# Kernel optimization log

Measured on AMD Instinct MI355X. Metric: run time of the kernel, lower is better.

Reference implementation:

```python
import jax, jax.numpy as jnp
import numpy as np

B, T, D = 4, 4096, 1024
H, K, V = 16, 64, 64
EPS = 1e-6


def setup_inputs() -> dict:
    key = jax.random.key(0)
    ks = jax.random.split(key, 7)
    s = 0.02
    return {
        "x": jax.random.normal(ks[0], (B, T, D), dtype=jnp.float32),
        "norm_w": jnp.ones((D,), dtype=jnp.float32),
        "Wk": jax.random.normal(ks[1], (H * K, D), dtype=jnp.float32) * s,
        "Wv": jax.random.normal(ks[2], (H * V, D), dtype=jnp.float32) * s,
        "Wo": jax.random.normal(ks[3], (D, H * V), dtype=jnp.float32) * s,
        "Wb": jax.random.normal(ks[4], (H, D), dtype=jnp.float32) * s,
        "bb": jnp.full((H,), -2.0, dtype=jnp.float32),
        "Wg": jax.random.normal(ks[5], (H, D), dtype=jnp.float32) * s,
        "bg": jnp.full((H,), 2.0, dtype=jnp.float32),
    }


def reference(x, norm_w, Wk, Wv, Wo, Wb, bb, Wg, bg):
    # RMSNorm
    rms = jnp.sqrt(jnp.mean(x * x, axis=-1, keepdims=True) + EPS)
    xn = x / rms * norm_w  # [B,T,D]

    k = (xn @ Wk.T).reshape(B, T, H, K)
    v = (xn @ Wv.T).reshape(B, T, H, V)
    # L2-normalize keys (F.normalize, eps=1e-12)
    kn = jnp.linalg.norm(k, axis=-1, keepdims=True)
    k = k / jnp.maximum(kn, 1e-12)

    beta = jax.nn.sigmoid(xn @ Wb.T + bb)  # [B,T,H]
    g = jax.nn.sigmoid(xn @ Wg.T + bg)     # [B,T,H]

    # time-major for scan
    k_t = jnp.transpose(k, (1, 0, 2, 3))       # [T,B,H,K]
    v_t = jnpp = jnp.transpose(v, (1, 0, 2, 3))  # [T,B,H,V]
    b_t = jnp.transpose(beta, (1, 0, 2))       # [T,B,H]
    g_t = jnp.transpose(g, (1, 0, 2))          # [T,B,H]

    state0 = jnp.zeros((B, H, K, V), dtype=jnp.float32)

    def step(state, inp):
        kt, vt, bt, gt = inp  # [B,H,K],[B,H,V],[B,H],[B,H]
        pred = jnp.einsum('bhkv,bhk->bhv', state, kt)
        err = vt - pred
        state = gt[..., None, None] * state + bt[..., None, None] * (kt[..., :, None] * err[..., None, :])
        out_t = jnp.einsum('bhkv,bhk->bhv', state, kt)
        return state, out_t

    final_state, out = jax.lax.scan(step, state0, (k_t, v_t, b_t, g_t))
    out = jnp.transpose(out, (1, 0, 2, 3)).reshape(B, T, H * V)  # [B,T,H*V]
    y = x + out @ Wo.T
    return y
```

## Files before the change

### kernel.cpp

```cpp
#include <hip/hip_runtime.h>
#include <stdint.h>

#define B_ 4
#define T_ 4096
#define D_ 1024
#define H_ 16
#define NPAD 2176
#define ROWS (B_*T_)

typedef __bf16 bf16x8 __attribute__((ext_vector_type(8)));
typedef float  f32x4  __attribute__((ext_vector_type(4)));
typedef unsigned short u16;
typedef u16 u16x8 __attribute__((ext_vector_type(8)));
typedef u16 u16x4 __attribute__((ext_vector_type(4)));

__device__ __forceinline__ float bf2f(u16 u){
  union { unsigned int i; float f; } x; x.i = ((unsigned int)u) << 16; return x.f;
}
__device__ __forceinline__ u16 f2bf(float f){
  union { float f; unsigned int i; } x; x.f = f;
  unsigned int r = x.i + 0x7fffu + ((x.i >> 16) & 1u);
  return (u16)(r >> 16);
}
__device__ __forceinline__ bf16x8 as_bf(u16x8 v){ union{u16x8 u; bf16x8 b;} x; x.u = v; return x.b; }

__device__ __forceinline__ void gload_lds16(const u16* g, u16* l){
  __builtin_amdgcn_global_load_lds(
      (const __attribute__((address_space(1))) unsigned int*)g,
      (__attribute__((address_space(3))) unsigned int*)l, 16, 0, 0);
}

__global__ __launch_bounds__(256) void prep_w(
    const float* __restrict__ Wk, const float* __restrict__ Wv,
    const float* __restrict__ Wb, const float* __restrict__ Wg,
    const float* __restrict__ Wo, u16* __restrict__ Wcomb, u16* __restrict__ Wob)
{
  long i = (long)blockIdx.x * 256 + threadIdx.x;
  const long tot1 = (long)NPAD * D_;
  if (i < tot1) {
    long n = i >> 10, d = i & 1023;
    float v;
    if      (n < 1024) v = Wk[n * 1024 + d];
    else if (n < 2048) v = Wv[(n - 1024) * 1024 + d];
    else if (n < 2064) v = Wb[(n - 2048) * 1024 + d];
    else if (n < 2080) v = Wg[(n - 2064) * 1024 + d];
    else               v = 0.f;
    Wcomb[i] = f2bf(v);
  } else {
    long j = i - tot1;
    Wob[j] = f2bf(Wo[j]);
  }
}

__global__ __launch_bounds__(256) void rmsnorm_k(
    const float* __restrict__ x, const float* __restrict__ w, u16* __restrict__ xn)
{
  long row = blockIdx.x;
  int tid = threadIdx.x;
  int l = tid & 63, wv = tid >> 6;
  f32x4 v = ((const f32x4*)(x + row * D_))[tid];
  float ss = v[0]*v[0] + v[1]*v[1] + v[2]*v[2] + v[3]*v[3];
  #pragma unroll
  for (int m = 1; m < 64; m <<= 1) ss += __shfl_xor(ss, m, 64);
  __shared__ float red[4];
  if (l == 0) red[wv] = ss;
  __syncthreads();
  float tot = red[0] + red[1] + red[2] + red[3];
  float inv = rsqrtf(tot * (1.f / (float)D_) + 1e-6f);
  f32x4 wv4 = ((const f32x4*)w)[tid];
  u16x4 o;
  o[0] = f2bf(v[0] * inv * wv4[0]);
  o[1] = f2bf(v[1] * inv * wv4[1]);
  o[2] = f2bf(v[2] * inv * wv4[2]);
  o[3] = f2bf(v[3] * inv * wv4[3]);
  ((u16x4*)(xn + row * D_))[tid] = o;
}

template<int RESID, int OUTF32>
__global__ __launch_bounds__(256) void gemm_nt(
    const u16* __restrict__ A, const u16* __restrict__ Bm,
    u16* __restrict__ Cb, float* __restrict__ Cf, const float* __restrict__ resid,
    int M, int N, int Kd)
{
  __shared__ __align__(16) u16 Als[128 * 32];
  __shared__ __align__(16) u16 Bls[128 * 32];
  const int tid = threadIdx.x;
  const int w = tid >> 6, l = tid & 63;
  const int wr = w >> 1, wc = w & 1;
  const int lm = l & 15, lq = l >> 4;

  unsigned bid = blockIdx.y * gridDim.x + blockIdx.x;
  unsigned nwg = gridDim.x * gridDim.y;
  unsigned cpx = nwg >> 3;
  unsigned swz = (bid & 7) * cpx + (bid >> 3);
  const long bm0 = (long)(swz / gridDim.x) * 128;
  const long bn0 = (long)(swz % gridDim.x) * 128;

  f32x4 zero4 = {0.f, 0.f, 0.f, 0.f};
  f32x4 acc[4][4];
  #pragma unroll
  for (int i = 0; i < 4; i++)
    #pragma unroll
    for (int j = 0; j < 4; j++) acc[i][j] = zero4;

  for (int kk = 0; kk < Kd; kk += 32) {
    __syncthreads();
    #pragma unroll
    for (int it = 0; it < 2; it++) {
      int c = tid + it * 256;
      int r = c >> 2, kb = c & 3;
      const u16* ga = A  + (bm0 + r) * Kd + kk + kb * 8;
      const u16* gb = Bm + (bn0 + r) * Kd + kk + kb * 8;
      gload_lds16(ga, Als + (it * 256 + w * 64) * 8);
      gload_lds16(gb, Bls + (it * 256 + w * 64) * 8);
    }
    __syncthreads();
    bf16x8 af[4], bfr[4];
    #pragma unroll
    for (int f = 0; f < 4; f++)
      af[f] = *(const bf16x8*)(Als + (wr * 64 + f * 16 + lm) * 32 + lq * 8);
    #pragma unroll
    for (int f = 0; f < 4; f++)
      bfr[f] = *(const bf16x8*)(Bls + (wc * 64 + f * 16 + lm) * 32 + lq * 8);
    #pragma unroll
    for (int i = 0; i < 4; i++)
      #pragma unroll
      for (int j = 0; j < 4; j++)
        acc[i][j] = __builtin_amdgcn_mfma_f32_16x16x32_bf16(af[i], bfr[j], acc[i][j], 0, 0, 0);
  }

  #pragma unroll
  for (int i = 0; i < 4; i++) {
    #pragma unroll
    for (int r = 0; r < 4; r++) {
      long m = bm0 + wr * 64 + i * 16 + lq * 4 + r;
      #pragma unroll
      for (int j = 0; j < 4; j++) {
        long n = bn0 + wc * 64 + j * 16 + lm;
        float val = acc[i][j][r];
        if (RESID) val += resid[m * N + n];
        if (OUTF32) Cf[m * N + n] = val;
        else        Cb[m * N + n] = f2bf(val);
      }
    }
  }
}

__global__ __launch_bounds__(64) void postproc(
    u16* __restrict__ kv, const float* __restrict__ bb, const float* __restrict__ bg,
    float* __restrict__ bArr, float* __restrict__ gArr)
{
  long row = blockIdx.x;
  int l = threadIdx.x;
  u16* rp = kv + row * NPAD;
  #pragma unroll
  for (int h = 0; h < 16; h++) {
    float xk = bf2f(rp[h * 64 + l]);
    float ss = xk * xk;
    #pragma unroll
    for (int m = 1; m < 64; m <<= 1) ss += __shfl_xor(ss, m, 64);
    float inv = 1.f / fmaxf(sqrtf(ss), 1e-12f);
    rp[h * 64 + l] = f2bf(xk * inv);
  }
  if (l < 32) {
    int hh = l & 15;
    float val = bf2f(rp[2048 + l]) + ((l < 16) ? bb[hh] : bg[hh]);
    float s = 1.f / (1.f + expf(-val));
    float* dst = (l < 16) ? bArr : gArr;
    long b = row >> 12;
    long t = row & 4095;
    dst[(b * H_ + hh) * (long)T_ + t] = s;
  }
}

__device__ __forceinline__ void mm64(const u16* Ab, const u16* Bb,
                                     int lm, int lq, int wr, int wc, f32x4 acc[2][2])
{
  #pragma unroll
  for (int ks = 0; ks < 2; ++ks) {
    bf16x8 af[2], bfr[2];
    #pragma unroll
    for (int mi = 0; mi < 2; ++mi)
      af[mi] = *(const bf16x8*)(Ab + (wr*32 + mi*16 + lm)*72 + ks*32 + lq*8);
    #pragma unroll
    for (int ni = 0; ni < 2; ++ni)
      bfr[ni] = *(const bf16x8*)(Bb + (wc*32 + ni*16 + lm)*72 + ks*32 + lq*8);
    #pragma unroll
    for (int mi = 0; mi < 2; ++mi)
      #pragma unroll
      for (int ni = 0; ni < 2; ++ni)
        acc[mi][ni] = __builtin_amdgcn_mfma_f32_16x16x32_bf16(af[mi], bfr[ni], acc[mi][ni], 0, 0, 0);
  }
}

__global__ __launch_bounds__(256) void chunk1(
    u16* __restrict__ kv, const float* __restrict__ bArr, const float* __restrict__ gArr,
    u16* __restrict__ p1buf, u16* __restrict__ r1buf)
{
  __shared__ __align__(16) u16 Kb[64*72];
  __shared__ __align__(16) u16 Utb[128*72];
  __shared__ __align__(16) u16 LpI[64*72];
  __shared__ __align__(16) u16 Abf[64*72];
  __shared__ __align__(16) float Ad[4*16*21];
  __shared__ float aLS[64], ainvLS[64], bLS[64], bapLS[64];
  __shared__ float aCsh;

  const int tid = threadIdx.x;
  const int w = tid >> 6, l = tid & 63;
  const int lm = l & 15, lq = l >> 4;
  const int wr = w >> 1, wc = w & 1;
  const int bh = blockIdx.x & 63, ch = blockIdx.x >> 6;
  const int b = bh >> 4, h = bh & 15;

  const u16* kbase = kv + ((long)b*T_ + ch*64)*NPAD + h*64;
  const u16* vbase = kbase + 1024;

  #pragma unroll
  for (int it = 0; it < 2; ++it) {
    int c = tid + it*256;
    int r = c >> 3, seg = (c & 7)*8;
    *(u16x8*)(Kb  + r*72 + seg) = *(const u16x8*)(kbase + (long)r*NPAD + seg);
    *(u16x8*)(Utb + r*72 + seg) = *(const u16x8*)(vbase + (long)r*NPAD + seg);
  }
  #pragma unroll
  for (int z = 0; z < 8; ++z) {
    int idx = tid + z*256;
    int rr = idx >> 5, wd = idx & 31;
    ((unsigned int*)(Utb + (64 + rr)*72))[wd] = 0u;
  }
  if (tid < 64) {
    float gv = gArr[(long)bh*T_ + ch*64 + tid];
    float bv = bArr[(long)bh*T_ + ch*64 + tid];
    float av = gv;
    #pragma unroll
    for (int off = 1; off < 64; off <<= 1) {
      float o = __shfl_up(av, off, 64);
      if (tid >= off) av *= o;
    }
    float ap = __shfl_up(av, 1, 64);
    if (tid == 0) ap = 1.f;
    float aC = __shfl(av, 63, 64);
    aLS[tid] = av; ainvLS[tid] = 1.f/av; bLS[tid] = bv; bapLS[tid] = bv*ap;
    if (tid == 0) aCsh = aC;
  }
  __syncthreads();

  f32x4 gf[2][2];
  #pragma unroll
  for (int mi = 0; mi < 2; ++mi)
    #pragma unroll
    for (int ni = 0; ni < 2; ++ni) gf[mi][ni] = f32x4{0.f,0.f,0.f,0.f};
  mm64(Kb, Kb, lm, lq, wr, wc, gf);

  float wv_[4][2][4];
  #pragma unroll
  for (int bi = 0; bi < 4; ++bi)
    #pragma unroll
    for (int ni = 0; ni < 2; ++ni) {
      int col = w*32 + ni*16 + lm;
      #pragma unroll
      for (int r = 0; r < 4; ++r) {
        int row = bi*16 + lq*4 + r;
        float sv = (col < 64) ? bf2f(Utb[row*72 + col]) : bf2f(Kb[row*72 + (col - 64)]);
        float coef = (col < 64) ? bLS[row] : bapLS[row];
        wv_[bi][ni][r] = coef * sv;
      }
    }

  #pragma unroll
  for (int mi = 0; mi < 2; ++mi)
    #pragma unroll
    for (int ni = 0; ni < 2; ++ni)
      #pragma unroll
      for (int r = 0; r < 4; ++r) {
        int row = wr*32 + mi*16 + lq*4 + r, col = wc*32 + ni*16 + lm;
        float gvl = gf[mi][ni][r];
        int rb = row >> 4, cb = col >> 4;
        Abf[row*72 + col] = f2bf((rb > cb) ? bapLS[row]*ainvLS[col]*gvl : 0.f);
        if (rb == cb)
          Ad[(rb*16 + (row & 15))*21 + (col & 15)] =
              ((col & 15) < (row & 15)) ? bapLS[row]*ainvLS[col]*gvl : 0.f;
        LpI[row*72 + col] = f2bf((col < row) ? aLS[row]*ainvLS[col]*gvl
                                             : ((col == row) ? 1.f : 0.f));
      }
  __syncthreads();

  #pragma unroll
  for (int bi = 0; bi < 4; ++bi) {
    if (bi > 0) {
      f32x4 corr[2] = { f32x4{0.f,0.f,0.f,0.f}, f32x4{0.f,0.f,0.f,0.f} };
      const int nks = (bi*16 + 31) >> 5;
      #pragma unroll
      for (int ks = 0; ks < 2; ++ks) {
        if (ks < nks) {
          bf16x8 afr = *(const bf16x8*)(Abf + (bi*16 + lm)*72 + ks*32 + lq*8);
          #pragma unroll
          for (int ni = 0; ni < 2; ++ni) {
            bf16x8 bfr = *(const bf16x8*)(Utb + (w*32 + ni*16 + lm)*72 + ks*32 + lq*8);
            corr[ni] = __builtin_amdgcn_mfma_f32_16x16x32_bf16(afr, bfr, corr[ni], 0, 0, 0);
          }
        }
      }
      #pragma unroll
      for (int ni = 0; ni < 2; ++ni)
        #pragma unroll
        for (int r = 0; r < 4; ++r) wv_[bi][ni][r] -= corr[ni][r];
    }
    #pragma unroll
    for (int i = 0; i < 16; ++i) {
      int src = ((i >> 2) << 4) | lm;
      float u0 = __shfl(wv_[bi][0][i & 3], src, 64);
      float u1 = __shfl(wv_[bi][1][i & 3], src, 64);
      #pragma unroll
      for (int r = 0; r < 4; ++r) {
        float ad = Ad[(bi*16 + lq*4 + r)*21 + i];
        wv_[bi][0][r] = fmaf(-ad, u0, wv_[bi][0][r]);
        wv_[bi][1][r] = fmaf(-ad, u1, wv_[bi][1][r]);
      }
    }
    #pragma unroll
    for (int ni = 0; ni < 2; ++ni) {
      int col = w*32 + ni*16 + lm;
      #pragma unroll
      for (int r = 0; r < 4; ++r)
        Utb[col*72 + bi*16 + lq*4 + r] = f2bf(wv_[bi][ni][r]);
    }
  }
  __syncthreads();

  const long pr_base = (((long)bh*64 + ch)*64);
  u16* qdst = kv + ((long)b*T_ + ch*64)*NPAD + h*64;
  u16* mdst = qdst + 1024;
  f32x4 acc[2][2];

  #pragma unroll
  for (int mi = 0; mi < 2; ++mi)
    #pragma unroll
    for (int ni = 0; ni < 2; ++ni) acc[mi][ni] = f32x4{0.f,0.f,0.f,0.f};
  mm64(Utb, LpI, lm, lq, wr, wc, acc);
  #pragma unroll
  for (int mi = 0; mi < 2; ++mi)
    #pragma unroll
    for (int ni = 0; ni < 2; ++ni)
      #pragma unroll
      for (int r = 0; r < 4; ++r) {
        int row = wr*32 + mi*16 + lq*4 + r, col = wc*32 + ni*16 + lm;
        p1buf[(pr_base + row)*64 + col] = f2bf(acc[mi][ni][r]);
      }

  #pragma unroll
  for (int mi = 0; mi < 2; ++mi)
    #pragma unroll
    for (int ni = 0; ni < 2; ++ni) acc[mi][ni] = f32x4{0.f,0.f,0.f,0.f};
  mm64(LpI, Utb + 64*72, lm, lq, wr, wc, acc);
  #pragma unroll
  for (int mi = 0; mi < 2; ++mi)
    #pragma unroll
    for (int ni = 0; ni < 2; ++ni)
      #pragma unroll
      for (int r = 0; r < 4; ++r) {
        int row = wr*32 + mi*16 + lq*4 + r, col = wc*32 + ni*16 + lm;
        float val = aLS[row]*bf2f(Kb[row*72 + col]) - acc[mi][ni][r];
        qdst[(long)row*NPAD + col] = f2bf(val);
      }

  {
    int kk_ = tid >> 2, sb = (tid & 3) * 16;
    float aC = aCsh;
    #pragma unroll
    for (int s5 = 0; s5 < 16; ++s5) {
      int s = sb + s5;
      Abf[kk_*72 + s] = f2bf(aC * ainvLS[s] * bf2f(Kb[s*72 + kk_]));
    }
  }
  __syncthreads();

  #pragma unroll
  for (int mi = 0; mi < 2; ++mi)
    #pragma unroll
    for (int ni = 0; ni < 2; ++ni) acc[mi][ni] = f32x4{0.f,0.f,0.f,0.f};
  mm64(Utb, Abf, lm, lq, wr, wc, acc);
  #pragma unroll
  for (int mi = 0; mi < 2; ++mi)
    #pragma unroll
    for (int ni = 0; ni < 2; ++ni)
      #pragma unroll
      for (int r = 0; r < 4; ++r) {
        int row = wr*32 + mi*16 + lq*4 + r, col = wc*32 + ni*16 + lm;
        r1buf[(pr_base + row)*64 + col] = f2bf(acc[mi][ni][r]);
      }

  #pragma unroll
  for (int mi = 0; mi < 2; ++mi)
    #pragma unroll
    for (int ni = 0; ni < 2; ++ni) acc[mi][ni] = f32x4{0.f,0.f,0.f,0.f};
  mm64(Abf, Utb + 64*72, lm, lq, wr, wc, acc);
  #pragma unroll
  for (int mi = 0; mi < 2; ++mi)
    #pragma unroll
    for (int ni = 0; ni < 2; ++ni)
      #pragma unroll
      for (int r = 0; r < 4; ++r) {
        int row = wr*32 + mi*16 + lq*4 + r, col = wc*32 + ni*16 + lm;
        float val = ((row == col) ? aCsh : 0.f) - acc[mi][ni][r];
        mdst[(long)row*NPAD + col] = f2bf(val);
      }
}

struct PF { u16x8 qf0, qf1, mf0, mf1; u16 p1[4]; u16 r1[4]; };

__global__ __launch_bounds__(256) void chunk2(
    const u16* __restrict__ kv, const u16* __restrict__ p1buf, const u16* __restrict__ r1buf,
    u16* __restrict__ outb)
{
  __shared__ __align__(16) u16 Zb[16*72];
  __shared__ __align__(16) u16 ot[64*24];
  const int tid = threadIdx.x;
  const int wcv = tid >> 6, l = tid & 63;
  const int lm = l & 15, lq = l >> 4;
  const int bh = blockIdx.x & 63, vg = blockIdx.x >> 6;
  const int b = bh >> 4, h = bh & 15;

  for (int idx = tid; idx < 16*72/2; idx += 256) ((unsigned int*)Zb)[idx] = 0u;

  const u16* pbase = p1buf + (long)bh*64*4096;
  const u16* rbase = r1buf + (long)bh*64*4096;

  auto LOADPF = [&](int ch, PF& p){
    long rq = ((long)b*T_ + ch*64 + wcv*16 + lm)*NPAD + h*64 + lq*8;
    p.qf0 = *(const u16x8*)(kv + rq);
    p.qf1 = *(const u16x8*)(kv + rq + 32);
    p.mf0 = *(const u16x8*)(kv + rq + 1024);
    p.mf1 = *(const u16x8*)(kv + rq + 1024 + 32);
    #pragma unroll
    for (int r = 0; r < 4; ++r) {
      long pv = (long)ch*4096 + (vg*16 + lq*4 + r)*64 + wcv*16 + lm;
      p.p1[r] = pbase[pv];
      p.r1[r] = rbase[pv];
    }
  };

  PF A, Bp;
  LOADPF(0, A);
  __syncthreads();

  auto STEP = [&](int ch, PF& use, PF& pre){
    bf16x8 za0 = *(const bf16x8*)(Zb + lm*72 + lq*8);
    bf16x8 za1 = *(const bf16x8*)(Zb + lm*72 + 32 + lq*8);
    if (ch < 63) LOADPF(ch + 1, pre);
    f32x4 accO = { bf2f(use.p1[0]), bf2f(use.p1[1]), bf2f(use.p1[2]), bf2f(use.p1[3]) };
    accO = __builtin_amdgcn_mfma_f32_16x16x32_bf16(za0, as_bf(use.qf0), accO, 0, 0, 0);
    accO = __builtin_amdgcn_mfma_f32_16x16x32_bf16(za1, as_bf(use.qf1), accO, 0, 0, 0);
    f32x4 accS = { bf2f(use.r1[0]), bf2f(use.r1[1]), bf2f(use.r1[2]), bf2f(use.r1[3]) };
    accS = __builtin_amdgcn_mfma_f32_16x16x32_bf16(za0, as_bf(use.mf0), accS, 0, 0, 0);
    accS = __builtin_amdgcn_mfma_f32_16x16x32_bf16(za1, as_bf(use.mf1), accS, 0, 0, 0);
    #pragma unroll
    for (int r = 0; r < 4; ++r) ot[(wcv*16 + lm)*24 + lq*4 + r] = f2bf(accO[r]);
    __syncthreads();
    #pragma unroll
    for (int r = 0; r < 4; ++r) Zb[(lq*4 + r)*72 + wcv*16 + lm] = f2bf(accS[r]);
    {
      int i2 = tid >> 2, q4 = tid & 3;
      u16x4 ov = *(const u16x4*)(ot + i2*24 + q4*4);
      *(u16x4*)(outb + ((long)b*T_ + ch*64 + i2)*D_ + h*64 + vg*16 + q4*4) = ov;
    }
    __syncthreads();
  };

  for (int c2 = 0; c2 < 32; ++c2) {
    STEP(2*c2,     A, Bp);
    STEP(2*c2 + 1, Bp, A);
  }
}

extern "C" void kernel_launch(void* const* d_in, const int* in_sizes, int n_in,
                              void* d_out, int out_size, void* d_ws, size_t ws_size,
                              hipStream_t stream) {
  const float* x     = (const float*)d_in[0];
  const float* normw = (const float*)d_in[1];
  const float* Wk    = (const float*)d_in[2];
  const float* Wv    = (const float*)d_in[3];
  const float* Wo    = (const float*)d_in[4];
  const float* Wb    = (const float*)d_in[5];
  const float* bb    = (const float*)d_in[6];
  const float* Wg    = (const float*)d_in[7];
  const float* bg    = (const float*)d_in[8];
  float* y = (float*)d_out;

  char* ws = (char*)d_ws;
  u16* xn    = (u16*)ws;   ws += (long)ROWS * D_ * 2;
  u16* Wcomb = (u16*)ws;   ws += (long)NPAD * D_ * 2;
  u16* Wob   = (u16*)ws;   ws += (long)D_ * D_ * 2;
  u16* kvb   = (u16*)ws;   ws += (long)ROWS * NPAD * 2;
  float* bA  = (float*)ws; ws += (long)B_ * H_ * T_ * 4;
  float* gA  = (float*)ws; ws += (long)B_ * H_ * T_ * 4;
  u16* outb  = (u16*)ws;   ws += (long)ROWS * D_ * 2;
  u16* r1b   = (u16*)ws;   ws += (long)64 * 64 * 4096 * 2;

  const long prep_total = (long)NPAD * D_ + (long)D_ * D_;
  prep_w<<<dim3((unsigned)(prep_total / 256)), dim3(256), 0, stream>>>(
      Wk, Wv, Wb, Wg, Wo, Wcomb, Wob);
  rmsnorm_k<<<dim3(ROWS), dim3(256), 0, stream>>>(x, normw, xn);
  gemm_nt<0, 0><<<dim3(NPAD / 128, ROWS / 128), dim3(256), 0, stream>>>(
      xn, Wcomb, kvb, (float*)nullptr, (const float*)nullptr, ROWS, NPAD, D_);
  postproc<<<dim3(ROWS), dim3(64), 0, stream>>>(kvb, bb, bg, bA, gA);
  chunk1<<<dim3(4096), dim3(256), 0, stream>>>(kvb, bA, gA, xn, r1b);
  chunk2<<<dim3(256), dim3(256), 0, stream>>>(kvb, xn, r1b, outb);
  gemm_nt<1, 1><<<dim3(D_ / 128, ROWS / 128), dim3(256), 0, stream>>>(
      outb, Wob, (u16*)nullptr, y, x, ROWS, D_, D_);
}
```

Baseline: 364.1 us.

## Add 256x256-tile triple-buffered GEMM with direct-to-LDS loads for projections

Introduces a 512-thread GEMM kernel with 256x256 output tiles, three LDS stages of async global-to-LDS loads, and the staging of A and B interleaved between two MFMA halves using s_setprio. It replaces the 128x128 GEMM for both the fused input projection and the output projection when 96KB of dynamic LDS can be requested. NPAD grows to 2304 so the projection width divides by 256, which adds padded columns of wasted compute and memory. Larger tiles raise arithmetic intensity and reuse, but the grids get smaller (e.g. 4x64 blocks for the output GEMM), which may underfill the CUs.

```diff
diff --git a/kernel.cpp b/kernel.cpp
--- a/kernel.cpp
+++ b/kernel.cpp
@@ -5,7 +5,7 @@
 #define T_ 4096
 #define D_ 1024
 #define H_ 16
-#define NPAD 2176
+#define NPAD 2304
 #define ROWS (B_*T_)
 
 typedef __bf16 bf16x8 __attribute__((ext_vector_type(8)));
@@ -76,6 +76,135 @@
   ((u16x4*)(xn + row * D_))[tid] = o;
 }
 
+extern __shared__ f32x4 lds_dyn[];
+
+template<int RESID, int OUTF32>
+__global__ __launch_bounds__(512, 2) void gemm256(
+    const u16* __restrict__ A, const u16* __restrict__ Bm,
+    u16* __restrict__ Cb, float* __restrict__ Cf, const float* __restrict__ resid,
+    int M, int N, int Kd)
+{
+  const int tid = threadIdx.x;
+  const int w = tid >> 6, l = tid & 63;
+  const int lm = l & 15, lq = l >> 4;
+  const int wm = w >> 2, wn = w & 3;
+
+  unsigned gx = gridDim.x;
+  unsigned bid = blockIdx.y * gx + blockIdx.x;
+  unsigned nwg = gx * gridDim.y;
+  unsigned cpx = nwg >> 3;
+  unsigned swz = (bid & 7) * cpx + (bid >> 3);
+  const long bm0 = (long)(swz / gx) * 256;
+  const long bn0 = (long)(swz % gx) * 256;
+
+  char* lds = (char*)lds_dyn;
+
+  int rowS[2], colS[2];
+  #pragma unroll
+  for (int r = 0; r < 2; ++r) {
+    int c = r*512 + w*64 + l;
+    int row = c >> 2, slot = c & 3;
+    rowS[r] = row;
+    colS[r] = (slot ^ (row & 3)) * 8;
+  }
+
+  auto STAGE_A = [&](int t, int q){
+    char* base = lds + q*32768;
+    long k0 = (long)t * 32;
+    #pragma unroll
+    for (int r = 0; r < 2; ++r)
+      gload_lds16(A + (bm0 + rowS[r])*(long)Kd + k0 + colS[r],
+                  (u16*)(base + (r*512 + w*64)*16));
+  };
+  auto STAGE_B = [&](int t, int q){
+    char* base = lds + q*32768 + 16384;
+    long k0 = (long)t * 32;
+    #pragma unroll
+    for (int r = 0; r < 2; ++r)
+      gload_lds16(Bm + (bn0 + rowS[r])*(long)Kd + k0 + colS[r],
+                  (u16*)(base + (r*512 + w*64)*16));
+  };
+
+  f32x4 acc[8][4];
+  #pragma unroll
+  for (int i = 0; i < 8; ++i)
+    #pragma unroll
+    for (int j = 0; j < 4; ++j) acc[i][j] = f32x4{0.f,0.f,0.f,0.f};
+
+  const int NT = Kd >> 5;
+  STAGE_A(0, 0); STAGE_B(0, 0);
+  STAGE_A(1, 1); STAGE_B(1, 1);
+
+  for (int t = 0; t < NT; ++t) {
+    int q  = t % 3;
+    int qn = (t + 2) % 3;
+    int tn = (t + 2 < NT) ? (t + 2) : (NT - 1);
+
+    asm volatile("s_waitcnt vmcnt(4)" ::: "memory");
+    __builtin_amdgcn_s_barrier();
+    asm volatile("" ::: "memory");
+
+    const char* Ab = lds + q*32768;
+    const char* Bb = Ab + 16384;
+
+    bf16x8 bfr[4];
+    #pragma unroll
+    for (int nf = 0; nf < 4; ++nf) {
+      int rr = wn*64 + nf*16 + lm;
+      bfr[nf] = *(const bf16x8*)(Bb + rr*64 + (((unsigned)lq << 4) ^ ((unsigned)(rr & 3) << 4)));
+    }
+    bf16x8 afr[4];
+    #pragma unroll
+    for (int mf = 0; mf < 4; ++mf) {
+      int rr = wm*128 + mf*16 + lm;
+      afr[mf] = *(const bf16x8*)(Ab + rr*64 + (((unsigned)lq << 4) ^ ((unsigned)(rr & 3) << 4)));
+    }
+    STAGE_A(tn, qn);
+
+    __builtin_amdgcn_s_setprio(1);
+    #pragma unroll
+    for (int mf = 0; mf < 4; ++mf)
+      #pragma unroll
+      for (int nf = 0; nf < 4; ++nf)
+        acc[mf][nf] = __builtin_amdgcn_mfma_f32_16x16x32_bf16(afr[mf], bfr[nf], acc[mf][nf], 0, 0, 0);
+    __builtin_amdgcn_s_setprio(0);
+
+    __builtin_amdgcn_s_barrier();
+    asm volatile("" ::: "memory");
+
+    #pragma unroll
+    for (int mf = 0; mf < 4; ++mf) {
+      int rr = wm*128 + 64 + mf*16 + lm;
+      afr[mf] = *(const bf16x8*)(Ab + rr*64 + (((unsigned)lq << 4) ^ ((unsigned)(rr & 3) << 4)));
+    }
+    STAGE_B(tn, qn);
+
+    __builtin_amdgcn_s_setprio(1);
+    #pragma unroll
+    for (int mf = 0; mf < 4; ++mf)
+      #pragma unroll
+      for (int nf = 0; nf < 4; ++nf)
+        acc[4+mf][nf] = __builtin_amdgcn_mfma_f32_16x16x32_bf16(afr[mf], bfr[nf], acc[4+mf][nf], 0, 0, 0);
+    __builtin_amdgcn_s_setprio(0);
+  }
+
+  #pragma unroll
+  for (int mf = 0; mf < 8; ++mf) {
+    #pragma unroll
+    for (int r = 0; r < 4; ++r) {
+      long m = bm0 + wm*128 + mf*16 + lq*4 + r;
+      #pragma unroll
+      for (int nf = 0; nf < 4; ++nf) {
+        long n = bn0 + wn*64 + nf*16 + lm;
+        float val = acc[mf][nf][r];
+        if (RESID) val += resid[m * N + n];
+        if (OUTF32) Cf[m * N + n] = val;
+        else        Cb[m * N + n] = f2bf(val);
+      }
+    }
+  }
+}
+
 template<int RESID, int OUTF32>
 __global__ __launch_bounds__(256) void gemm_nt(
     const u16* __restrict__ A, const u16* __restrict__ Bm,
@@ -497,15 +626,30 @@
   u16* outb  = (u16*)ws;   ws += (long)ROWS * D_ * 2;
   u16* r1b   = (u16*)ws;   ws += (long)64 * 64 * 4096 * 2;
 
+  const int LDSB = 3 * 32768;
+  bool big = true;
+  if (hipFuncSetAttribute(reinterpret_cast<const void*>(gemm256<0,0>),
+        hipFuncAttributeMaxDynamicSharedMemorySize, LDSB) != hipSuccess) big = false;
+  if (hipFuncSetAttribute(reinterpret_cast<const void*>(gemm256<1,1>),
+        hipFuncAttributeMaxDynamicSharedMemorySize, LDSB) != hipSuccess) big = false;
+
   const long prep_total = (long)NPAD * D_ + (long)D_ * D_;
   prep_w<<<dim3((unsigned)(prep_total / 256)), dim3(256), 0, stream>>>(
       Wk, Wv, Wb, Wg, Wo, Wcomb, Wob);
   rmsnorm_k<<<dim3(ROWS), dim3(256), 0, stream>>>(x, normw, xn);
-  gemm_nt<0, 0><<<dim3(NPAD / 128, ROWS / 128), dim3(256), 0, stream>>>(
-      xn, Wcomb, kvb, (float*)nullptr, (const float*)nullptr, ROWS, NPAD, D_);
+  if (big)
+    gemm256<0, 0><<<dim3(NPAD / 256, ROWS / 256), dim3(512), LDSB, stream>>>(
+        xn, Wcomb, kvb, (float*)nullptr, (const float*)nullptr, ROWS, NPAD, D_);
+  else
+    gemm_nt<0, 0><<<dim3(NPAD / 128, ROWS / 128), dim3(256), 0, stream>>>(
+        xn, Wcomb, kvb, (float*)nullptr, (const float*)nullptr, ROWS, NPAD, D_);
   postproc<<<dim3(ROWS), dim3(64), 0, stream>>>(kvb, bb, bg, bA, gA);
   chunk1<<<dim3(4096), dim3(256), 0, stream>>>(kvb, bA, gA, xn, r1b);
   chunk2<<<dim3(256), dim3(256), 0, stream>>>(kvb, xn, r1b, outb);
-  gemm_nt<1, 1><<<dim3(D_ / 128, ROWS / 128), dim3(256), 0, stream>>>(
-      outb, Wob, (u16*)nullptr, y, x, ROWS, D_, D_);
-}
+  if (big)
+    gemm256<1, 1><<<dim3(D_ / 256, ROWS / 256), dim3(512), LDSB, stream>>>(
+        outb, Wob, (u16*)nullptr, y, x, ROWS, D_, D_);
+  else
+    gemm_nt<1, 1><<<dim3(D_ / 128, ROWS / 128), dim3(256), 0, stream>>>(
+        outb, Wob, (u16*)nullptr, y, x, ROWS, D_, D_);
+}
```

New measurement: 348.8 us. 1.04x faster.
